# Kernel optimization log

Hardware: AMD Instinct MI355X
Metric: run time of the kernel (lower is better)

The kernel has to match this reference:

```python
import jax, jax.numpy as jnp
import numpy as np

NUM_ITER = 3
NUM_BINS = 10
MAX_DISP = 4
BIN_DISP = 0.5
CHANNELS = 32
MIN_FILTER_REG = 1e-05
SEARCH = 2 * MAX_DISP + 1
CORR_CH = SEARCH * SEARCH  # 81


def local_cost_volume(f1, f2, d):
    """uflow-style local cost volume: mean over channels of f1 * shifted f2.
    f1, f2: (B,H,W,C) -> (B,H,W,(2d+1)^2)."""
    B, H, W, C = f1.shape
    f2p = jnp.pad(f2, ((0, 0), (d, d), (d, d), (0, 0)))
    s = 2 * d + 1
    cols = [jnp.mean(f1 * f2p[:, i:i + H, j:j + W, :], axis=-1)
            for i in range(s) for j in range(s)]
    return jnp.stack(cols, axis=-1)


def compute_distance_map():
    # (1, SEARCH, SEARCH, NUM_BINS) soft-binned displacement distances
    bins = jnp.arange(NUM_BINS, dtype=jnp.float32).reshape(1, 1, 1, NUM_BINS)
    disp = jnp.arange(-MAX_DISP, MAX_DISP + 1, dtype=jnp.float32)
    k0 = disp.reshape(1, SEARCH, 1, 1)
    k1 = disp.reshape(1, 1, SEARCH, 1)
    dist = jnp.sqrt(k0 * k0 + k1 * k1)
    bin_diff = dist / BIN_DISP - bins
    # faithful to source: slice along axis=1 (spatial rows), as written in TF code
    bin_val = jnp.concatenate(
        [jax.nn.relu(1.0 - jnp.abs(bin_diff[:, :-1, :, :])),
         jnp.clip(1.0 + bin_diff[:, -1:, :, :], 0.0, 1.0)], axis=1)
    return bin_val


def leaky_par(x, a):
    return (1.0 - a) / 2.0 * jnp.abs(x) + (1.0 + a) / 2.0 * x


def leaky_par_deriv(x, a):
    return (1.0 - a) / 2.0 * jnp.sign(jax.lax.stop_gradient(x)) + (1.0 + a) / 2.0


def setup_inputs() -> dict:
    key = jax.random.key(0)
    ks = jax.random.split(key, 4)
    B, H, W, C = 4, 256, 256, CHANNELS
    d = jnp.arange(NUM_BINS, dtype=jnp.float32) * BIN_DISP
    gauss = jnp.exp(-0.5 * d * d)  # init_gauss_sigma = 1.0
    return {
        "reference_feature": jax.random.normal(ks[0], (B, H, W, C), jnp.float32),
        "query_feature": jax.random.normal(ks[1], (B, H, W, C), jnp.float32),
        "beta": jnp.ones((1,), jnp.float32),
        "target_map_w": gauss - jnp.min(gauss),                 # (NUM_BINS,)
        "spatial_w": jnp.ones((NUM_BINS,), jnp.float32),        # (NUM_BINS,)
        "mask_w": 4.0 * jnp.tanh(2.0 - d),                      # (NUM_BINS,)
        "mr_w": jax.random.normal(ks[2], (CORR_CH, CHANNELS), jnp.float32) * 0.05,
        "mr_b": jnp.zeros((CHANNELS,), jnp.float32),
        "lr_w": jax.random.normal(ks[3], (CORR_CH, CHANNELS), jnp.float32) * 0.05,
        "lr_b": jnp.zeros((CHANNELS,), jnp.float32),
        "w_reg": 0.01 * jnp.ones((1,), jnp.float32),
        "log_step_length": jnp.zeros((1,), jnp.float32),
    }


def reference(reference_feature, query_feature, beta, target_map_w, spatial_w,
              mask_w, mr_w, mr_b, lr_w, lr_b, w_reg, log_step_length):
    C = reference_feature.shape[-1]
    # filter initializer: beta * feat / (mean(feat^2) + eps)
    w = beta * reference_feature / (
        jnp.mean(reference_feature * reference_feature, axis=-1, keepdims=True) + 1e-06)
    reg_weight = jnp.clip(w_reg * w_reg, MIN_FILTER_REG ** 2 / C ** 2, None)
    step_length = jnp.exp(log_step_length)

    dm = compute_distance_map()                     # (1,9,9,NUM_BINS)
    y = jnp.einsum('ahwb,b->ahw', dm, target_map_w).reshape(1, 1, 1, -1)       # (1,1,1,81)
    v_plus = jnp.einsum('ahwb,b->ahw', dm, spatial_w).reshape(1, 1, 1, -1)     # (1,1,1,81)
    weight_m = jax.nn.sigmoid(jnp.einsum('ahwb,b->ahw', dm, mask_w)).reshape(1, 1, 1, -1)

    for _ in range(NUM_ITER):
        c = local_cost_volume(w, reference_feature, MAX_DISP)        # (B,H,W,81)
        act = v_plus * leaky_par(c, weight_m)
        dact = v_plus * leaky_par_deriv(c, weight_m)
        res = act - v_plus * y
        mapped = jnp.einsum('bhwk,kc->bhwc', dact * res, mr_w) + mr_b  # 81 -> 32
        fg_loss = jnp.einsum('bhwk,kc->bhwc',
                             local_cost_volume(mapped, reference_feature, MAX_DISP),
                             lr_w) + lr_b                              # 81 -> 32
        filter_grad = reg_weight * w + fg_loss
        scores = dact * local_cost_volume(filter_grad, reference_feature, MAX_DISP)
        alpha_den = jnp.sum(scores * scores, axis=-1, keepdims=True)
        alpha_num = jnp.sum(filter_grad * filter_grad, axis=-1, keepdims=True)
        alpha = alpha_num / alpha_den
        w = w + alpha * step_length * filter_grad
    return w
```

## Files before the change

### kernel.cpp

```cpp
#include <hip/hip_runtime.h>

#define B_ 4
#define H_ 256
#define W_ 256
#define PXF4 9

__device__ __forceinline__ float dot32f(const float* a, const float4* r) {
    float s0 = 0.f, s1 = 0.f, s2 = 0.f, s3 = 0.f;
#pragma unroll
    for (int u = 0; u < 8; ++u) {
        float4 q = r[u];
        s0 += a[4*u+0] * q.x; s1 += a[4*u+1] * q.y;
        s2 += a[4*u+2] * q.z; s3 += a[4*u+3] * q.w;
    }
    return (s0 + s1) + (s2 + s3);
}

template<int TSX, int TSY, int NTH>
__global__ void __launch_bounds__(NTH)
gocor(const float* __restrict__ rf_g,
      const float* __restrict__ beta_p, const float* __restrict__ tw_p,
      const float* __restrict__ sw_p,  const float* __restrict__ mw_p,
      const float* __restrict__ mrw_p, const float* __restrict__ mrb_p,
      const float* __restrict__ lrw_p, const float* __restrict__ lrb_p,
      const float* __restrict__ wreg_p, const float* __restrict__ lsl_p,
      float* __restrict__ out)
{
    constexpr int TWXc = TSX + 8, TWYc = TSY + 8, NPXc = TWXc * TWYc;
    extern __shared__ float4 smem[];
    float4* s_rf  = smem;
    float4* s_kp  = smem + NPXc * PXF4;
    float*  s_bias = (float*)(s_kp + 81);

    const int tid = threadIdx.x;
    const int tx = tid % TSX, ty = tid / TSX;
    const int bx = blockIdx.x * TSX, by = blockIdx.y * TSY, bb = blockIdx.z;
    const float* rfb = rf_g + (size_t)bb * H_ * W_ * 32;

    for (int idx = tid; idx < NPXc * 8; idx += NTH) {
        int u = idx & 7, p = idx >> 3;
        int ly = p / TWXc, lx = p - ly * TWXc;
        int gy = by + ly - 4, gx = bx + lx - 4;
        float4 v = make_float4(0.f, 0.f, 0.f, 0.f);
        if (gy >= 0 && gy < H_ && gx >= 0 && gx < W_)
            v = *(const float4*)(rfb + ((size_t)(gy * W_ + gx)) * 32 + u * 4);
        s_rf[p * PXF4 + u] = v;
    }

    if (tid < 81) {
        int i = tid / 9, j = tid % 9;
        float di = (float)(i - 4), dj = (float)(j - 4);
        float dist = sqrtf(di * di + dj * dj);
        float y = 0.f, vp = 0.f, m = 0.f;
        for (int b = 0; b < 10; ++b) {
            float bd = 2.f * dist - (float)b;
            float val;
            if (i < 8) val = fmaxf(0.f, 1.f - fabsf(bd));
            else       val = fminf(1.f, fmaxf(0.f, 1.f + bd));
            y  += val * tw_p[b];
            vp += val * sw_p[b];
            m  += val * mw_p[b];
        }
        float wm = 1.f / (1.f + expf(-m));
        s_kp[tid] = make_float4(vp * 0.5f * (1.f - wm),
                                vp * 0.5f * (1.f + wm),
                                vp * y, 0.f);
    }
    if (tid < 32)      s_bias[tid]      = mrb_p[tid];
    else if (tid < 64) s_bias[tid]      = lrb_p[tid - 32];

    float beta = beta_p[0];
    float wr   = wreg_p[0];
    float regw = fmaxf(wr * wr, (1e-5f * 1e-5f) / (32.f * 32.f));
    float step = expf(lsl_p[0]);

    __syncthreads();

    float w[32];
    {
        const float4* r = &s_rf[(((ty + 4) * TWXc) + (tx + 4)) * PXF4];
#pragma unroll
        for (int u = 0; u < 8; ++u) {
            float4 q = r[u];
            w[4*u+0] = q.x; w[4*u+1] = q.y; w[4*u+2] = q.z; w[4*u+3] = q.w;
        }
        float msq = 0.f;
#pragma unroll
        for (int c = 0; c < 32; ++c) msq += w[c] * w[c];
        float inv = beta / (msq * (1.f / 32.f) + 1e-6f);
#pragma unroll
        for (int c = 0; c < 32; ++c) w[c] *= inv;
    }

    float mp[32], fg[32];

    for (int it = 0; it < 3; ++it) {
        unsigned long long sp0 = 0ull, sn0 = 0ull;
        unsigned int sp1 = 0u, sn1 = 0u;
#pragma unroll
        for (int c = 0; c < 32; ++c) mp[c] = s_bias[c];
        for (int i = 0; i < 9; ++i) {
            int rowbase = (ty + i) * TWXc + tx;
            for (int j = 0; j < 9; ++j) {
                int k = i * 9 + j;
                const float4* r = &s_rf[(rowbase + j) * PXF4];
                float ck = dot32f(w, r) * (1.f / 32.f);
                if (ck > 0.f)      { if (k < 64) sp0 |= 1ull << k; else sp1 |= 1u << (k - 64); }
                else if (ck < 0.f) { if (k < 64) sn0 |= 1ull << k; else sn1 |= 1u << (k - 64); }
                float4 kp = s_kp[k];
                float sg = (ck > 0.f) ? 1.f : ((ck < 0.f) ? -1.f : 0.f);
                float act  = kp.x * fabsf(ck) + kp.y * ck;
                float res  = act - kp.z;
                float dact = kp.x * sg + kp.y;
                float s = dact * res;
                const float* mr = mrw_p + k * 32;
#pragma unroll
                for (int c = 0; c < 32; ++c) mp[c] += s * mr[c];
            }
        }

#pragma unroll
        for (int c = 0; c < 32; ++c) fg[c] = s_bias[32 + c] + regw * w[c];
        for (int i = 0; i < 9; ++i) {
            int rowbase = (ty + i) * TWXc + tx;
            for (int j = 0; j < 9; ++j) {
                int k = i * 9 + j;
                const float4* r = &s_rf[(rowbase + j) * PXF4];
                float ck = dot32f(mp, r) * (1.f / 32.f);
                const float* lr = lrw_p + k * 32;
#pragma unroll
                for (int c = 0; c < 32; ++c) fg[c] += ck * lr[c];
            }
        }

        float num = 0.f;
#pragma unroll
        for (int c = 0; c < 32; ++c) num += fg[c] * fg[c];
        float den = 0.f;
        for (int i = 0; i < 9; ++i) {
            int rowbase = (ty + i) * TWXc + tx;
            for (int j = 0; j < 9; ++j) {
                int k = i * 9 + j;
                const float4* r = &s_rf[(rowbase + j) * PXF4];
                float c3 = dot32f(fg, r) * (1.f / 32.f);
                bool bp = (k < 64) ? ((sp0 >> k) & 1ull) : ((sp1 >> (k - 64)) & 1u);
                bool bn = (k < 64) ? ((sn0 >> k) & 1ull) : ((sn1 >> (k - 64)) & 1u);
                float sg = bp ? 1.f : (bn ? -1.f : 0.f);
                float4 kp = s_kp[k];
                float dact = kp.x * sg + kp.y;
                float s3 = dact * c3;
                den += s3 * s3;
            }
        }
        float as = (num / den) * step;
#pragma unroll
        for (int c = 0; c < 32; ++c) w[c] += as * fg[c];
    }

    float* o = out + (((size_t)bb * H_ + (by + ty)) * W_ + (bx + tx)) * 32;
#pragma unroll
    for (int u = 0; u < 8; ++u)
        *(float4*)(o + u * 4) = make_float4(w[4*u+0], w[4*u+1], w[4*u+2], w[4*u+3]);
}

static const size_t BIG_SHM   = (size_t)(40 * 24 * PXF4 + 81 + 16) * 16;
static const size_t SMALL_SHM = (size_t)(24 * 16 * PXF4 + 81 + 16) * 16;

static bool query_big_path() {
    int dev = 0;
    if (hipGetDevice(&dev) != hipSuccess) return false;
    hipFuncSetAttribute(reinterpret_cast<const void*>(&gocor<32, 16, 512>),
                        hipFuncAttributeMaxDynamicSharedMemorySize, (int)BIG_SHM);
    int maxShm = 0;
    if (hipDeviceGetAttribute(&maxShm, hipDeviceAttributeMaxSharedMemoryPerBlock, dev) == hipSuccess &&
        (size_t)maxShm >= BIG_SHM)
        return true;
    hipFuncAttributes fa;
    if (hipFuncGetAttributes(&fa, reinterpret_cast<const void*>(&gocor<32, 16, 512>)) == hipSuccess &&
        (size_t)fa.maxDynamicSharedSizeBytes >= BIG_SHM)
        return true;
    return false;
}

extern "C" void kernel_launch(void* const* d_in, const int* in_sizes, int n_in,
                              void* d_out, int out_size, void* d_ws, size_t ws_size,
                              hipStream_t stream) {
    (void)d_ws; (void)ws_size; (void)in_sizes; (void)n_in; (void)out_size;
    static const bool use_big = query_big_path();

    const float* rf   = (const float*)d_in[0];
    const float* beta = (const float*)d_in[2];
    const float* tw   = (const float*)d_in[3];
    const float* sw   = (const float*)d_in[4];
    const float* mw   = (const float*)d_in[5];
    const float* mrw  = (const float*)d_in[6];
    const float* mrb  = (const float*)d_in[7];
    const float* lrw  = (const float*)d_in[8];
    const float* lrb  = (const float*)d_in[9];
    const float* wreg = (const float*)d_in[10];
    const float* lsl  = (const float*)d_in[11];
    float* o = (float*)d_out;

    if (use_big) {
        dim3 grid(W_ / 32, H_ / 16, B_);
        hipLaunchKernelGGL((gocor<32, 16, 512>), grid, dim3(512), BIG_SHM, stream,
                           rf, beta, tw, sw, mw, mrw, mrb, lrw, lrb, wreg, lsl, o);
    } else {
        dim3 grid(W_ / 16, H_ / 8, B_);
        hipLaunchKernelGGL((gocor<16, 8, 128>), grid, dim3(128), SMALL_SHM, stream,
                           rf, beta, tw, sw, mw, mrw, mrb, lrw, lrb, wreg, lsl, o);
    }
}
```

Before: 678.2 us.

## Compute two vertically adjacent pixels per thread to reuse shared-memory neighbor loads

The big-tile kernel now uses 256 threads, and each thread handles two vertically stacked pixels. Each thread walks 10 rows of the 9-wide window, so every loaded reference-feature vector feeds both pixels' dot products in all three phases. This roughly halves LDS traffic per pixel. The cost is doubled register arrays (w, mp, fg for two pixels, about 192 floats live), which raises register pressure and may cut occupancy or cause spills.

After: 1.109 ms. +63.5%, slower.

```diff
diff --git a/kernel.cpp b/kernel.cpp
--- a/kernel.cpp
+++ b/kernel.cpp
@@ -5,41 +5,75 @@
 #define W_ 256
 #define PXF4 9
 
-__device__ __forceinline__ float dot32f(const float* a, const float4* r) {
+__device__ __forceinline__ float dot32q(const float* a, const float4* q) {
     float s0 = 0.f, s1 = 0.f, s2 = 0.f, s3 = 0.f;
 #pragma unroll
     for (int u = 0; u < 8; ++u) {
-        float4 q = r[u];
-        s0 += a[4*u+0] * q.x; s1 += a[4*u+1] * q.y;
-        s2 += a[4*u+2] * q.z; s3 += a[4*u+3] * q.w;
+        float4 v = q[u];
+        s0 += a[4*u+0] * v.x; s1 += a[4*u+1] * v.y;
+        s2 += a[4*u+2] * v.z; s3 += a[4*u+3] * v.w;
     }
     return (s0 + s1) + (s2 + s3);
 }
 
-template<int TSX, int TSY, int NTH>
-__global__ void __launch_bounds__(NTH)
-gocor(const float* __restrict__ rf_g,
-      const float* __restrict__ beta_p, const float* __restrict__ tw_p,
-      const float* __restrict__ sw_p,  const float* __restrict__ mw_p,
-      const float* __restrict__ mrw_p, const float* __restrict__ mrb_p,
-      const float* __restrict__ lrw_p, const float* __restrict__ lrb_p,
-      const float* __restrict__ wreg_p, const float* __restrict__ lsl_p,
-      float* __restrict__ out)
+struct Signs { unsigned long long p0, n0; unsigned int p1, n1; };
+
+__device__ __forceinline__ void phaseA_step(float ck, int k, const float4* s_kp,
+                                            const float* __restrict__ mrw_p,
+                                            float* mp, Signs& sg) {
+    if (ck > 0.f)      { if (k < 64) sg.p0 |= 1ull << k; else sg.p1 |= 1u << (k - 64); }
+    else if (ck < 0.f) { if (k < 64) sg.n0 |= 1ull << k; else sg.n1 |= 1u << (k - 64); }
+    float4 kp = s_kp[k];
+    float sn = (ck > 0.f) ? 1.f : ((ck < 0.f) ? -1.f : 0.f);
+    float act  = kp.x * fabsf(ck) + kp.y * ck;
+    float res  = act - kp.z;
+    float dact = kp.x * sn + kp.y;
+    float s = dact * res;
+    const float* mr = mrw_p + k * 32;
+#pragma unroll
+    for (int c = 0; c < 32; ++c) mp[c] += s * mr[c];
+}
+
+__device__ __forceinline__ void phaseC_step(float c3, int k, const float4* s_kp,
+                                            const Signs& sg, float& den) {
+    bool bp = (k < 64) ? ((sg.p0 >> k) & 1ull) : ((sg.p1 >> (k - 64)) & 1u);
+    bool bn = (k < 64) ? ((sg.n0 >> k) & 1ull) : ((sg.n1 >> (k - 64)) & 1u);
+    float sn = bp ? 1.f : (bn ? -1.f : 0.f);
+    float4 kp = s_kp[k];
+    float dact = kp.x * sn + kp.y;
+    float s3 = dact * c3;
+    den += s3 * s3;
+}
+
+#define TSX2 32
+#define TSY2 16
+#define TWX2 40
+#define TWY2 24
+#define NPX2 (TWX2 * TWY2)
+
+__global__ void __launch_bounds__(256)
+gocor2(const float* __restrict__ rf_g,
+       const float* __restrict__ beta_p, const float* __restrict__ tw_p,
+       const float* __restrict__ sw_p,  const float* __restrict__ mw_p,
+       const float* __restrict__ mrw_p, const float* __restrict__ mrb_p,
+       const float* __restrict__ lrw_p, const float* __restrict__ lrb_p,
+       const float* __restrict__ wreg_p, const float* __restrict__ lsl_p,
+       float* __restrict__ out)
 {
-    constexpr int TWXc = TSX + 8, TWYc = TSY + 8, NPXc = TWXc * TWYc;
     extern __shared__ float4 smem[];
-    float4* s_rf  = smem;
-    float4* s_kp  = smem + NPXc * PXF4;
+    float4* s_rf   = smem;
+    float4* s_kp   = smem + NPX2 * PXF4;
     float*  s_bias = (float*)(s_kp + 81);
 
     const int tid = threadIdx.x;
-    const int tx = tid % TSX, ty = tid / TSX;
-    const int bx = blockIdx.x * TSX, by = blockIdx.y * TSY, bb = blockIdx.z;
+    const int tx = tid & 31, tyh = tid >> 5;
+    const int ty0 = tyh * 2;
+    const int bx = blockIdx.x * TSX2, by = blockIdx.y * TSY2, bb = blockIdx.z;
     const float* rfb = rf_g + (size_t)bb * H_ * W_ * 32;
 
-    for (int idx = tid; idx < NPXc * 8; idx += NTH) {
+    for (int idx = tid; idx < NPX2 * 8; idx += 256) {
         int u = idx & 7, p = idx >> 3;
-        int ly = p / TWXc, lx = p - ly * TWXc;
+        int ly = p / TWX2, lx = p - ly * TWX2;
         int gy = by + ly - 4, gx = bx + lx - 4;
         float4 v = make_float4(0.f, 0.f, 0.f, 0.f);
         if (gy >= 0 && gy < H_ && gx >= 0 && gx < W_)
@@ -66,8 +100,8 @@
                                 vp * 0.5f * (1.f + wm),
                                 vp * y, 0.f);
     }
-    if (tid < 32)      s_bias[tid]      = mrb_p[tid];
-    else if (tid < 64) s_bias[tid]      = lrb_p[tid - 32];
+    if (tid < 32)      s_bias[tid] = mrb_p[tid];
+    else if (tid < 64) s_bias[tid] = lrb_p[tid - 32];
 
     float beta = beta_p[0];
     float wr   = wreg_p[0];
@@ -76,6 +110,167 @@
 
     __syncthreads();
 
+    float w0[32], w1[32];
+    {
+#pragma unroll
+        for (int px = 0; px < 2; ++px) {
+            float* w = px ? w1 : w0;
+            const float4* r = &s_rf[(((ty0 + px + 4) * TWX2) + (tx + 4)) * PXF4];
+#pragma unroll
+            for (int u = 0; u < 8; ++u) {
+                float4 q = r[u];
+                w[4*u+0] = q.x; w[4*u+1] = q.y; w[4*u+2] = q.z; w[4*u+3] = q.w;
+            }
+            float msq = 0.f;
+#pragma unroll
+            for (int c = 0; c < 32; ++c) msq += w[c] * w[c];
+            float inv = beta / (msq * (1.f / 32.f) + 1e-6f);
+#pragma unroll
+            for (int c = 0; c < 32; ++c) w[c] *= inv;
+        }
+    }
+
+    float mp0[32], mp1[32], fg0[32], fg1[32];
+
+    for (int it = 0; it < 3; ++it) {
+        Signs sg0{0ull, 0ull, 0u, 0u}, sg1{0ull, 0ull, 0u, 0u};
+#pragma unroll
+        for (int c = 0; c < 32; ++c) { mp0[c] = s_bias[c]; mp1[c] = s_bias[c]; }
+        for (int r = 0; r < 10; ++r) {
+            const float4* rowp = &s_rf[((ty0 + r) * TWX2 + tx) * PXF4];
+            for (int j = 0; j < 9; ++j) {
+                float4 q[8];
+                const float4* src = rowp + j * PXF4;
+#pragma unroll
+                for (int u = 0; u < 8; ++u) q[u] = src[u];
+                if (r < 9) phaseA_step(dot32q(w0, q) * (1.f / 32.f), r * 9 + j,
+                                       s_kp, mrw_p, mp0, sg0);
+                if (r > 0) phaseA_step(dot32q(w1, q) * (1.f / 32.f), (r - 1) * 9 + j,
+                                       s_kp, mrw_p, mp1, sg1);
+            }
+        }
+
+#pragma unroll
+        for (int c = 0; c < 32; ++c) {
+            fg0[c] = s_bias[32 + c] + regw * w0[c];
+            fg1[c] = s_bias[32 + c] + regw * w1[c];
+        }
+        for (int r = 0; r < 10; ++r) {
+            const float4* rowp = &s_rf[((ty0 + r) * TWX2 + tx) * PXF4];
+            for (int j = 0; j < 9; ++j) {
+                float4 q[8];
+                const float4* src = rowp + j * PXF4;
+#pragma unroll
+                for (int u = 0; u < 8; ++u) q[u] = src[u];
+                if (r < 9) {
+                    float ck = dot32q(mp0, q) * (1.f / 32.f);
+                    const float* lr = lrw_p + (r * 9 + j) * 32;
+#pragma unroll
+                    for (int c = 0; c < 32; ++c) fg0[c] += ck * lr[c];
+                }
+                if (r > 0) {
+                    float ck = dot32q(mp1, q) * (1.f / 32.f);
+                    const float* lr = lrw_p + ((r - 1) * 9 + j) * 32;
+#pragma unroll
+                    for (int c = 0; c < 32; ++c) fg1[c] += ck * lr[c];
+                }
+            }
+        }
+
+        float num0 = 0.f, num1 = 0.f;
+#pragma unroll
+        for (int c = 0; c < 32; ++c) { num0 += fg0[c] * fg0[c]; num1 += fg1[c] * fg1[c]; }
+        float den0 = 0.f, den1 = 0.f;
+        for (int r = 0; r < 10; ++r) {
+            const float4* rowp = &s_rf[((ty0 + r) * TWX2 + tx) * PXF4];
+            for (int j = 0; j < 9; ++j) {
+                float4 q[8];
+                const float4* src = rowp + j * PXF4;
+#pragma unroll
+                for (int u = 0; u < 8; ++u) q[u] = src[u];
+                if (r < 9) phaseC_step(dot32q(fg0, q) * (1.f / 32.f), r * 9 + j,
+                                       s_kp, sg0, den0);
+                if (r > 0) phaseC_step(dot32q(fg1, q) * (1.f / 32.f), (r - 1) * 9 + j,
+                                       s_kp, sg1, den1);
+            }
+        }
+        float as0 = (num0 / den0) * step, as1 = (num1 / den1) * step;
+#pragma unroll
+        for (int c = 0; c < 32; ++c) { w0[c] += as0 * fg0[c]; w1[c] += as1 * fg1[c]; }
+    }
+
+#pragma unroll
+    for (int px = 0; px < 2; ++px) {
+        const float* w = px ? w1 : w0;
+        float* o = out + (((size_t)bb * H_ + (by + ty0 + px)) * W_ + (bx + tx)) * 32;
+#pragma unroll
+        for (int u = 0; u < 8; ++u)
+            *(float4*)(o + u * 4) = make_float4(w[4*u+0], w[4*u+1], w[4*u+2], w[4*u+3]);
+    }
+}
+
+__device__ __forceinline__ float dot32f(const float* a, const float4* r) {
+    float s0 = 0.f, s1 = 0.f, s2 = 0.f, s3 = 0.f;
+#pragma unroll
+    for (int u = 0; u < 8; ++u) {
+        float4 q = r[u];
+        s0 += a[4*u+0] * q.x; s1 += a[4*u+1] * q.y;
+        s2 += a[4*u+2] * q.z; s3 += a[4*u+3] * q.w;
+    }
+    return (s0 + s1) + (s2 + s3);
+}
+
+__global__ void __launch_bounds__(128)
+gocor1(const float* __restrict__ rf_g,
+       const float* __restrict__ beta_p, const float* __restrict__ tw_p,
+       const float* __restrict__ sw_p,  const float* __restrict__ mw_p,
+       const float* __restrict__ mrw_p, const float* __restrict__ mrb_p,
+       const float* __restrict__ lrw_p, const float* __restrict__ lrb_p,
+       const float* __restrict__ wreg_p, const float* __restrict__ lsl_p,
+       float* __restrict__ out)
+{
+    constexpr int TWXc = 24, NPXc = 24 * 16;
+    extern __shared__ float4 smem[];
+    float4* s_rf  = smem;
+    float4* s_kp  = smem + NPXc * PXF4;
+    float*  s_bias = (float*)(s_kp + 81);
+
+    const int tid = threadIdx.x;
+    const int tx = tid & 15, ty = tid >> 4;
+    const int bx = blockIdx.x * 16, by = blockIdx.y * 8, bb = blockIdx.z;
+    const float* rfb = rf_g + (size_t)bb * H_ * W_ * 32;
+
+    for (int idx = tid; idx < NPXc * 8; idx += 128) {
+        int u = idx & 7, p = idx >> 3;
+        int ly = p / TWXc, lx = p - ly * TWXc;
+        int gy = by + ly - 4, gx = bx + lx - 4;
+        float4 v = make_float4(0.f, 0.f, 0.f, 0.f);
+        if (gy >= 0 && gy < H_ && gx >= 0 && gx < W_)
+            v = *(const float4*)(rfb + ((size_t)(gy * W_ + gx)) * 32 + u * 4);
+        s_rf[p * PXF4 + u] = v;
+    }
+    if (tid < 81) {
+        int i = tid / 9, j = tid % 9;
+        float di = (float)(i - 4), dj = (float)(j - 4);
+        float dist = sqrtf(di * di + dj * dj);
+        float y = 0.f, vp = 0.f, m = 0.f;
+        for (int b = 0; b < 10; ++b) {
+            float bd = 2.f * dist - (float)b;
+            float val = (i < 8) ? fmaxf(0.f, 1.f - fabsf(bd))
+                                : fminf(1.f, fmaxf(0.f, 1.f + bd));
+            y += val * tw_p[b]; vp += val * sw_p[b]; m += val * mw_p[b];
+        }
+        float wm = 1.f / (1.f + expf(-m));
+        s_kp[tid] = make_float4(vp * 0.5f * (1.f - wm), vp * 0.5f * (1.f + wm), vp * y, 0.f);
+    }
+    if (tid < 32)      s_bias[tid] = mrb_p[tid];
+    else if (tid < 64) s_bias[tid] = lrb_p[tid - 32];
+
+    float beta = beta_p[0], wr = wreg_p[0];
+    float regw = fmaxf(wr * wr, (1e-5f * 1e-5f) / (32.f * 32.f));
+    float step = expf(lsl_p[0]);
+    __syncthreads();
+
     float w[32];
     {
         const float4* r = &s_rf[(((ty + 4) * TWXc) + (tx + 4)) * PXF4];
@@ -93,90 +288,61 @@
     }
 
     float mp[32], fg[32];
-
     for (int it = 0; it < 3; ++it) {
-        unsigned long long sp0 = 0ull, sn0 = 0ull;
-        unsigned int sp1 = 0u, sn1 = 0u;
+        Signs sg{0ull, 0ull, 0u, 0u};
 #pragma unroll
         for (int c = 0; c < 32; ++c) mp[c] = s_bias[c];
         for (int i = 0; i < 9; ++i) {
             int rowbase = (ty + i) * TWXc + tx;
-            for (int j = 0; j < 9; ++j) {
-                int k = i * 9 + j;
-                const float4* r = &s_rf[(rowbase + j) * PXF4];
-                float ck = dot32f(w, r) * (1.f / 32.f);
-                if (ck > 0.f)      { if (k < 64) sp0 |= 1ull << k; else sp1 |= 1u << (k - 64); }
-                else if (ck < 0.f) { if (k < 64) sn0 |= 1ull << k; else sn1 |= 1u << (k - 64); }
-                float4 kp = s_kp[k];
-                float sg = (ck > 0.f) ? 1.f : ((ck < 0.f) ? -1.f : 0.f);
-                float act  = kp.x * fabsf(ck) + kp.y * ck;
-                float res  = act - kp.z;
-                float dact = kp.x * sg + kp.y;
-                float s = dact * res;
-                const float* mr = mrw_p + k * 32;
-#pragma unroll
-                for (int c = 0; c < 32; ++c) mp[c] += s * mr[c];
-            }
-        }
-
+            for (int j = 0; j < 9; ++j)
+                phaseA_step(dot32f(w, &s_rf[(rowbase + j) * PXF4]) * (1.f / 32.f),
+                            i * 9 + j, s_kp, mrw_p, mp, sg);
+        }
 #pragma unroll
         for (int c = 0; c < 32; ++c) fg[c] = s_bias[32 + c] + regw * w[c];
         for (int i = 0; i < 9; ++i) {
             int rowbase = (ty + i) * TWXc + tx;
             for (int j = 0; j < 9; ++j) {
-                int k = i * 9 + j;
-                const float4* r = &s_rf[(rowbase + j) * PXF4];
-                float ck = dot32f(mp, r) * (1.f / 32.f);
-                const float* lr = lrw_p + k * 32;
+                float ck = dot32f(mp, &s_rf[(rowbase + j) * PXF4]) * (1.f / 32.f);
+                const float* lr = lrw_p + (i * 9 + j) * 32;
 #pragma unroll
                 for (int c = 0; c < 32; ++c) fg[c] += ck * lr[c];
             }
         }
-
         float num = 0.f;
 #pragma unroll
         for (int c = 0; c < 32; ++c) num += fg[c] * fg[c];
         float den = 0.f;
         for (int i = 0; i < 9; ++i) {
             int rowbase = (ty + i) * TWXc + tx;
-            for (int j = 0; j < 9; ++j) {
-                int k = i * 9 + j;
-                const float4* r = &s_rf[(rowbase + j) * PXF4];
-                float c3 = dot32f(fg, r) * (1.f / 32.f);
-                bool bp = (k < 64) ? ((sp0 >> k) & 1ull) : ((sp1 >> (k - 64)) & 1u);
-                bool bn = (k < 64) ? ((sn0 >> k) & 1ull) : ((sn1 >> (k - 64)) & 1u);
-                float sg = bp ? 1.f : (bn ? -1.f : 0.f);
-                float4 kp = s_kp[k];
-                float dact = kp.x * sg + kp.y;
-                float s3 = dact * c3;
-                den += s3 * s3;
-            }
+            for (int j = 0; j < 9; ++j)
+                phaseC_step(dot32f(fg, &s_rf[(rowbase + j) * PXF4]) * (1.f / 32.f),
+                            i * 9 + j, s_kp, sg, den);
         }
         float as = (num / den) * step;
 #pragma unroll
         for (int c = 0; c < 32; ++c) w[c] += as * fg[c];
     }
-
     float* o = out + (((size_t)bb * H_ + (by + ty)) * W_ + (bx + tx)) * 32;
 #pragma unroll
     for (int u = 0; u < 8; ++u)
         *(float4*)(o + u * 4) = make_float4(w[4*u+0], w[4*u+1], w[4*u+2], w[4*u+3]);
 }
 
-static const size_t BIG_SHM   = (size_t)(40 * 24 * PXF4 + 81 + 16) * 16;
+static const size_t BIG_SHM   = (size_t)(NPX2 * PXF4 + 81 + 16) * 16;
 static const size_t SMALL_SHM = (size_t)(24 * 16 * PXF4 + 81 + 16) * 16;
 
 static bool query_big_path() {
     int dev = 0;
     if (hipGetDevice(&dev) != hipSuccess) return false;
-    hipFuncSetAttribute(reinterpret_cast<const void*>(&gocor<32, 16, 512>),
+    hipFuncSetAttribute(reinterpret_cast<const void*>(&gocor2),
                         hipFuncAttributeMaxDynamicSharedMemorySize, (int)BIG_SHM);
     int maxShm = 0;
     if (hipDeviceGetAttribute(&maxShm, hipDeviceAttributeMaxSharedMemoryPerBlock, dev) == hipSuccess &&
         (size_t)maxShm >= BIG_SHM)
         return true;
     hipFuncAttributes fa;
-    if (hipFuncGetAttributes(&fa, reinterpret_cast<const void*>(&gocor<32, 16, 512>)) == hipSuccess &&
+    if (hipFuncGetAttributes(&fa, reinterpret_cast<const void*>(&gocor2)) == hipSuccess &&
         (size_t)fa.maxDynamicSharedSizeBytes >= BIG_SHM)
         return true;
     return false;
@@ -202,12 +368,12 @@
     float* o = (float*)d_out;
 
     if (use_big) {
-        dim3 grid(W_ / 32, H_ / 16, B_);
-        hipLaunchKernelGGL((gocor<32, 16, 512>), grid, dim3(512), BIG_SHM, stream,
+        dim3 grid(W_ / TSX2, H_ / TSY2, B_);
+        hipLaunchKernelGGL(gocor2, grid, dim3(256), BIG_SHM, stream,
                            rf, beta, tw, sw, mw, mrw, mrb, lrw, lrb, wreg, lsl, o);
     } else {
         dim3 grid(W_ / 16, H_ / 8, B_);
-        hipLaunchKernelGGL((gocor<16, 8, 128>), grid, dim3(128), SMALL_SHM, stream,
+        hipLaunchKernelGGL(gocor1, grid, dim3(128), SMALL_SHM, stream,
                            rf, beta, tw, sw, mw, mrw, mrb, lrw, lrb, wreg, lsl, o);
     }
 }
```
